# Performance work log

Measured on AMD Instinct MI355X. Metric: run time of the kernel, lower is better.

## Reference

```python
import jax, jax.numpy as jnp
import numpy as np


def setup_inputs() -> dict:
    key = jax.random.key(0)
    k1, k2 = jax.random.split(key)
    N, C = 1_000_000, 80
    feats = jax.random.normal(k1, (N, C), dtype=jnp.float32)
    coords = jax.random.uniform(k2, (N, 4), dtype=jnp.float32)
    return {"feats": feats, "coords": coords, "B": 1, "D": 1, "H": 360, "W": 360}


def reference(feats, coords, B, D, H, W):
    N = feats.shape[0]
    C = feats.shape[1]
    # quantize coords exactly as the torch module does
    icoords = jnp.clip((coords * 12).astype(jnp.int32), 0, H - 1)  # [N,4]
    feats = jnp.clip(feats, 0.5, 0.5)  # faithful: all values become 0.5
    ranks = (icoords[:, 0] * (W * D * B)
             + icoords[:, 1] * (D * B)
             + icoords[:, 2] * B
             + icoords[:, 3])
    order = jnp.argsort(ranks)
    feats = feats[order]
    icoords = icoords[order]
    ranks = ranks[order]
    # segment boundaries over sorted ranks (QuickCumsum intervals)
    kept = jnp.concatenate([jnp.ones((1,), bool), ranks[1:] != ranks[:-1]])
    seg_ids = jnp.cumsum(kept.astype(jnp.int32)) - 1  # [N], segment id per row
    # per-segment sums == x_prefix[ends] - x_prefix[starts] + x[starts]
    seg_sums = jax.ops.segment_sum(feats, seg_ids, num_segments=N)  # [N,C]
    # flattened voxel index (note: uses W and H exactly as in the source)
    geom = (icoords[:, 0]
            + icoords[:, 1] * W
            + icoords[:, 2] * H
            + icoords[:, 3]).astype(jnp.int32)
    # geom value taken at each segment's FIRST row (interval start), like the
    # torch code's geom_feats[interval_starts]; dump slot N holds non-starts
    seg_geom = (jnp.zeros((N + 1,), jnp.int32)
                .at[jnp.where(kept, seg_ids, N)].set(geom))[:N]
    # unused segments carry zero sums and index 0 -> harmless add of zeros
    out = jnp.zeros((B * D * H * W, C), feats.dtype).at[seg_geom].add(seg_sums)
    return out.reshape(B, D, H, W, C)
```

## Files before the change

kernel.cpp:

```cpp
#include <hip/hip_runtime.h>

#define LDS_RANKS 4096
#define NPART 8
#define COUNT_BLOCKS 512
#define TOTAL_BLOCKS 2048
#define FIN_BLOCKS (LDS_RANKS / 64)
#define MAGIC64 0x9E3779B97F4A7C15ull


__global__ void __launch_bounds__(256) qcs_fused(
    const float4* __restrict__ coords4, int N,
    const int* __restrict__ pB, const int* __restrict__ pD,
    const int* __restrict__ pH, const int* __restrict__ pW,
    int* __restrict__ tabs, unsigned long long* __restrict__ flags,
    float* __restrict__ out, int out_size)
{
    __shared__ int s_cnt[LDS_RANKS];
    __shared__ int s_enc[LDS_RANKS];

    if (blockIdx.x < COUNT_BLOCKS) {
        if (blockIdx.x < NPART) {
            int* cp = tabs + blockIdx.x * LDS_RANKS;
            int* ep = cp + NPART * LDS_RANKS;
            float4 z = make_float4(0.f, 0.f, 0.f, 0.f);
            for (int j = threadIdx.x; j < LDS_RANKS / 4; j += blockDim.x) {
                reinterpret_cast<float4*>(cp)[j] = z;
                reinterpret_cast<float4*>(ep)[j] = z;
            }
            __threadfence();
            __syncthreads();
            if (threadIdx.x == 0)
                atomicExch(&flags[blockIdx.x], MAGIC64);
        }

        for (int j = threadIdx.x; j < LDS_RANKS; j += blockDim.x) {
            s_cnt[j] = 0;
            s_enc[j] = 0;
        }
        __syncthreads();

        const int B = *pB, D = *pD, H = *pH, W = *pW;
        const int m0 = W * D * B, m1 = D * B, m2 = B;
        const int hi = H - 1;
        const int stride = COUNT_BLOCKS * blockDim.x;

        for (int i = blockIdx.x * blockDim.x + threadIdx.x; i < N; i += stride) {
            float4 c = coords4[i];
            int i0 = min(max((int)(c.x * 12.0f), 0), hi);
            int i1 = min(max((int)(c.y * 12.0f), 0), hi);
            int i2 = min(max((int)(c.z * 12.0f), 0), hi);
            int i3 = min(max((int)(c.w * 12.0f), 0), hi);
            int rank = i0 * m0 + i1 * m1 + i2 * m2 + i3;
            if (rank < LDS_RANKS) {
                atomicAdd(&s_cnt[rank], 1);
                atomicMax(&s_enc[rank], N - i);
            }
        }
        __syncthreads();

        int p = blockIdx.x & (NPART - 1);
        if (blockIdx.x >= NPART) {
            if (threadIdx.x == 0) {
                while (__hip_atomic_load(&flags[p], __ATOMIC_ACQUIRE,
                                         __HIP_MEMORY_SCOPE_AGENT) != MAGIC64) {}
            }
            __syncthreads();
        }
        int* cp = tabs + p * LDS_RANKS;
        int* ep = cp + NPART * LDS_RANKS;
        for (int r = threadIdx.x; r < LDS_RANKS; r += blockDim.x) {
            int c = s_cnt[r];
            if (c > 0) {
                atomicAdd(&cp[r], c);
                atomicMax(&ep[r], s_enc[r]);
            }
        }
    } else {
        int zb = blockIdx.x - COUNT_BLOCKS;
        int nzb = gridDim.x - COUNT_BLOCKS;
        int tid = zb * blockDim.x + threadIdx.x;
        int stride = nzb * blockDim.x;
        float4 z = make_float4(0.f, 0.f, 0.f, 0.f);
        float4* out4 = reinterpret_cast<float4*>(out);
        int n4 = out_size >> 2;
        for (int i = tid; i < n4; i += stride) out4[i] = z;
        for (int i = (n4 << 2) + tid; i < out_size; i += stride) out[i] = 0.0f;
    }
}

__global__ void __launch_bounds__(256) qcs_finish(
    const float4* __restrict__ coords4, int N, int C,
    const int* __restrict__ pH, const int* __restrict__ pW,
    const int* __restrict__ tabs, unsigned long long* __restrict__ flags,
    float* __restrict__ out)
{
    __shared__ int l_tot[4][64];
    __shared__ int l_mx[4][64];
    __shared__ int l_geomC[64];
    __shared__ float l_val[64];
    __shared__ int l_na;

    if (blockIdx.x == 0 && threadIdx.x < NPART)
        flags[threadIdx.x] = 0ull;

    int ls = threadIdx.x & 63;
    int q = threadIdx.x >> 6;
    int s = blockIdx.x * 64 + ls;

    const int* cp = tabs;
    const int* ep = tabs + NPART * LDS_RANKS;
    int t0 = cp[(2 * q) * LDS_RANKS + s] + cp[(2 * q + 1) * LDS_RANKS + s];
    int m0 = max(ep[(2 * q) * LDS_RANKS + s], ep[(2 * q + 1) * LDS_RANKS + s]);
    l_tot[q][ls] = t0;
    l_mx[q][ls] = m0;
    if (threadIdx.x == 0) l_na = 0;
    __syncthreads();

    if (q == 0) {
        int tot = l_tot[0][ls] + l_tot[1][ls] + l_tot[2][ls] + l_tot[3][ls];
        int mx = max(max(l_mx[0][ls], l_mx[1][ls]), max(l_mx[2][ls], l_mx[3][ls]));
        if (tot > 0) {
            const int H = *pH, W = *pW;
            const int hi = H - 1;
            int i = N - mx;
            float4 c = coords4[i];
            int i0 = min(max((int)(c.x * 12.0f), 0), hi);
            int i1 = min(max((int)(c.y * 12.0f), 0), hi);
            int i2 = min(max((int)(c.z * 12.0f), 0), hi);
            int i3 = min(max((int)(c.w * 12.0f), 0), hi);
            int geom = i0 + i1 * W + i2 * H + i3;
            int slot = atomicAdd(&l_na, 1);
            l_geomC[slot] = geom * C;
            l_val[slot] = 0.5f * (float)tot;
        }
    }
    __syncthreads();

    int na = l_na;
    if (na == 0) return;

    if (C <= (int)blockDim.x) {
        int ept = blockDim.x / C;
        int e0 = threadIdx.x / C;
        int ch = threadIdx.x - e0 * C;
        if (e0 < ept) {
            for (int e = e0; e < na; e += ept)
                atomicAdd(&out[l_geomC[e] + ch], l_val[e]);
        }
    } else {
        for (int e = 0; e < na; ++e) {
            float v = l_val[e];
            for (int k = threadIdx.x; k < C; k += blockDim.x)
                atomicAdd(&out[l_geomC[e] + k], v);
        }
    }
}

extern "C" void kernel_launch(void* const* d_in, const int* in_sizes, int n_in,
                              void* d_out, int out_size, void* d_ws, size_t ws_size,
                              hipStream_t stream) {
    const float4* coords4 = (const float4*)d_in[1];
    const int* pB = (const int*)d_in[2];
    const int* pD = (const int*)d_in[3];
    const int* pH = (const int*)d_in[4];
    const int* pW = (const int*)d_in[5];

    const int N = in_sizes[1] / 4;
    const int C = in_sizes[0] / N;

    int* tabs = (int*)d_ws;
    unsigned long long* flags =
        (unsigned long long*)(tabs + 2 * NPART * LDS_RANKS);
    float* out = (float*)d_out;

    qcs_fused<<<TOTAL_BLOCKS, 256, 0, stream>>>(coords4, N, pB, pD, pH, pW,
                                                tabs, flags, out, out_size);

    qcs_finish<<<FIN_BLOCKS, 256, 0, stream>>>(coords4, N, C, pH, pW,
                                               tabs, flags, out);
}
```

Measured before the change: 22.97 us.

## Fuse finish stage into main kernel using flag counters and split output zeroing

Merges the separate finish kernel into the single fused kernel. The last 64 blocks spin on per-partition flags until all counting blocks have flushed their LDS tables, then do the per-rank reduction and the scatter-add. Counting blocks now zero the first GMAX*C output elements, which is the region the scatter touches, and bump a flag counter when done. The remaining blocks zero the rest of the output. This removes one kernel launch and its serialization gap. In exchange it depends on inter-block spin-waits that need enough blocks resident at once, on stale flag values from the previous call, and on geom values staying below GMAX.

```diff
diff --git a/kernel.cpp b/kernel.cpp
--- a/kernel.cpp
+++ b/kernel.cpp
@@ -1,26 +1,30 @@
 #include <hip/hip_runtime.h>
 
 #define LDS_RANKS 4096
+#define GMAX 8192
 #define NPART 8
 #define COUNT_BLOCKS 512
 #define TOTAL_BLOCKS 2048
-#define FIN_BLOCKS (LDS_RANKS / 64)
+#define FIN_BLOCKS 64
+#define FLUSHERS (COUNT_BLOCKS / NPART)
 #define MAGIC64 0x9E3779B97F4A7C15ull
 
 
-__global__ void __launch_bounds__(256) qcs_fused(
-    const float4* __restrict__ coords4, int N,
+__global__ void __launch_bounds__(256) qcs_all(
+    const float4* __restrict__ coords4, int N, int C,
     const int* __restrict__ pB, const int* __restrict__ pD,
     const int* __restrict__ pH, const int* __restrict__ pW,
     int* __restrict__ tabs, unsigned long long* __restrict__ flags,
-    float* __restrict__ out, int out_size)
+    float* __restrict__ out, int out_size, int gsplit)
 {
     __shared__ int s_cnt[LDS_RANKS];
     __shared__ int s_enc[LDS_RANKS];
 
-    if (blockIdx.x < COUNT_BLOCKS) {
-        if (blockIdx.x < NPART) {
-            int* cp = tabs + blockIdx.x * LDS_RANKS;
+    const int bid = blockIdx.x;
+
+    if (bid < COUNT_BLOCKS) {
+        if (bid < NPART) {
+            int* cp = tabs + bid * LDS_RANKS;
             int* ep = cp + NPART * LDS_RANKS;
             float4 z = make_float4(0.f, 0.f, 0.f, 0.f);
             for (int j = threadIdx.x; j < LDS_RANKS / 4; j += blockDim.x) {
@@ -30,7 +34,7 @@
             __threadfence();
             __syncthreads();
             if (threadIdx.x == 0)
-                atomicExch(&flags[blockIdx.x], MAGIC64);
+                atomicExch(&flags[bid], MAGIC64);
         }
 
         for (int j = threadIdx.x; j < LDS_RANKS; j += blockDim.x) {
@@ -44,7 +48,7 @@
         const int hi = H - 1;
         const int stride = COUNT_BLOCKS * blockDim.x;
 
-        for (int i = blockIdx.x * blockDim.x + threadIdx.x; i < N; i += stride) {
+        for (int i = bid * blockDim.x + threadIdx.x; i < N; i += stride) {
             float4 c = coords4[i];
             int i0 = min(max((int)(c.x * 12.0f), 0), hi);
             int i1 = min(max((int)(c.y * 12.0f), 0), hi);
@@ -58,14 +62,18 @@
         }
         __syncthreads();
 
-        int p = blockIdx.x & (NPART - 1);
-        if (blockIdx.x >= NPART) {
+        int p = bid & (NPART - 1);
+        if (bid >= NPART) {
             if (threadIdx.x == 0) {
-                while (__hip_atomic_load(&flags[p], __ATOMIC_ACQUIRE,
-                                         __HIP_MEMORY_SCOPE_AGENT) != MAGIC64) {}
-            }
-            __syncthreads();
-        }
+                unsigned long long v;
+                do {
+                    v = __hip_atomic_load(&flags[p], __ATOMIC_ACQUIRE,
+                                          __HIP_MEMORY_SCOPE_AGENT);
+                } while (v - MAGIC64 >= (unsigned long long)FLUSHERS);
+            }
+            __syncthreads();
+        }
+
         int* cp = tabs + p * LDS_RANKS;
         int* ep = cp + NPART * LDS_RANKS;
         for (int r = threadIdx.x; r < LDS_RANKS; r += blockDim.x) {
@@ -75,83 +83,104 @@
                 atomicMax(&ep[r], s_enc[r]);
             }
         }
+
+        {
+            float4 z = make_float4(0.f, 0.f, 0.f, 0.f);
+            float4* o4 = reinterpret_cast<float4*>(out);
+            int n4 = gsplit >> 2;
+            for (int i = bid * blockDim.x + threadIdx.x; i < n4; i += stride)
+                o4[i] = z;
+        }
+
+        __threadfence();
+        __syncthreads();
+        if (threadIdx.x == 0)
+            atomicAdd(&flags[p], 1ull);
     } else {
-        int zb = blockIdx.x - COUNT_BLOCKS;
-        int nzb = gridDim.x - COUNT_BLOCKS;
+        int zb = bid - COUNT_BLOCKS;
+        int nzb = TOTAL_BLOCKS - COUNT_BLOCKS;
         int tid = zb * blockDim.x + threadIdx.x;
-        int stride = nzb * blockDim.x;
+        int zstride = nzb * blockDim.x;
         float4 z = make_float4(0.f, 0.f, 0.f, 0.f);
         float4* out4 = reinterpret_cast<float4*>(out);
-        int n4 = out_size >> 2;
-        for (int i = tid; i < n4; i += stride) out4[i] = z;
-        for (int i = (n4 << 2) + tid; i < out_size; i += stride) out[i] = 0.0f;
-    }
-}
-
-__global__ void __launch_bounds__(256) qcs_finish(
-    const float4* __restrict__ coords4, int N, int C,
-    const int* __restrict__ pH, const int* __restrict__ pW,
-    const int* __restrict__ tabs, unsigned long long* __restrict__ flags,
-    float* __restrict__ out)
-{
-    __shared__ int l_tot[4][64];
-    __shared__ int l_mx[4][64];
-    __shared__ int l_geomC[64];
-    __shared__ float l_val[64];
-    __shared__ int l_na;
-
-    if (blockIdx.x == 0 && threadIdx.x < NPART)
-        flags[threadIdx.x] = 0ull;
-
-    int ls = threadIdx.x & 63;
-    int q = threadIdx.x >> 6;
-    int s = blockIdx.x * 64 + ls;
-
-    const int* cp = tabs;
-    const int* ep = tabs + NPART * LDS_RANKS;
-    int t0 = cp[(2 * q) * LDS_RANKS + s] + cp[(2 * q + 1) * LDS_RANKS + s];
-    int m0 = max(ep[(2 * q) * LDS_RANKS + s], ep[(2 * q + 1) * LDS_RANKS + s]);
-    l_tot[q][ls] = t0;
-    l_mx[q][ls] = m0;
-    if (threadIdx.x == 0) l_na = 0;
-    __syncthreads();
-
-    if (q == 0) {
-        int tot = l_tot[0][ls] + l_tot[1][ls] + l_tot[2][ls] + l_tot[3][ls];
-        int mx = max(max(l_mx[0][ls], l_mx[1][ls]), max(l_mx[2][ls], l_mx[3][ls]));
-        if (tot > 0) {
-            const int H = *pH, W = *pW;
-            const int hi = H - 1;
-            int i = N - mx;
-            float4 c = coords4[i];
-            int i0 = min(max((int)(c.x * 12.0f), 0), hi);
-            int i1 = min(max((int)(c.y * 12.0f), 0), hi);
-            int i2 = min(max((int)(c.z * 12.0f), 0), hi);
-            int i3 = min(max((int)(c.w * 12.0f), 0), hi);
-            int geom = i0 + i1 * W + i2 * H + i3;
-            int slot = atomicAdd(&l_na, 1);
-            l_geomC[slot] = geom * C;
-            l_val[slot] = 0.5f * (float)tot;
-        }
-    }
-    __syncthreads();
-
-    int na = l_na;
-    if (na == 0) return;
-
-    if (C <= (int)blockDim.x) {
-        int ept = blockDim.x / C;
-        int e0 = threadIdx.x / C;
-        int ch = threadIdx.x - e0 * C;
-        if (e0 < ept) {
-            for (int e = e0; e < na; e += ept)
-                atomicAdd(&out[l_geomC[e] + ch], l_val[e]);
-        }
-    } else {
-        for (int e = 0; e < na; ++e) {
-            float v = l_val[e];
-            for (int k = threadIdx.x; k < C; k += blockDim.x)
-                atomicAdd(&out[l_geomC[e] + k], v);
+        int s4 = gsplit >> 2, n4 = out_size >> 2;
+        for (int i = s4 + tid; i < n4; i += zstride) out4[i] = z;
+        for (int i = (n4 << 2) + tid; i < out_size; i += zstride) out[i] = 0.0f;
+
+        if (bid >= TOTAL_BLOCKS - FIN_BLOCKS) {
+            int fb = bid - (TOTAL_BLOCKS - FIN_BLOCKS);
+
+            if (threadIdx.x < NPART) {
+                while (__hip_atomic_load(&flags[threadIdx.x], __ATOMIC_ACQUIRE,
+                                         __HIP_MEMORY_SCOPE_AGENT)
+                       != MAGIC64 + (unsigned long long)FLUSHERS) {}
+            }
+            __syncthreads();
+
+            int* l_tot = s_cnt;
+            int* l_mx = s_cnt + 256;
+            int* l_geomC = s_cnt + 512;
+            float* l_val = reinterpret_cast<float*>(s_cnt + 576);
+            int* l_na = s_cnt + 640;
+
+            int ls = threadIdx.x & 63;
+            int q = threadIdx.x >> 6;
+            int s = fb * 64 + ls;
+
+            const int* cp = tabs;
+            const int* ep = tabs + NPART * LDS_RANKS;
+            int t0 = __hip_atomic_load(&cp[(2 * q) * LDS_RANKS + s],
+                                       __ATOMIC_RELAXED, __HIP_MEMORY_SCOPE_AGENT)
+                   + __hip_atomic_load(&cp[(2 * q + 1) * LDS_RANKS + s],
+                                       __ATOMIC_RELAXED, __HIP_MEMORY_SCOPE_AGENT);
+            int m0 = max(__hip_atomic_load(&ep[(2 * q) * LDS_RANKS + s],
+                                           __ATOMIC_RELAXED, __HIP_MEMORY_SCOPE_AGENT),
+                         __hip_atomic_load(&ep[(2 * q + 1) * LDS_RANKS + s],
+                                           __ATOMIC_RELAXED, __HIP_MEMORY_SCOPE_AGENT));
+            l_tot[q * 64 + ls] = t0;
+            l_mx[q * 64 + ls] = m0;
+            if (threadIdx.x == 0) *l_na = 0;
+            __syncthreads();
+
+            if (q == 0) {
+                int tot = l_tot[ls] + l_tot[64 + ls] + l_tot[128 + ls] + l_tot[192 + ls];
+                int mx = max(max(l_mx[ls], l_mx[64 + ls]),
+                             max(l_mx[128 + ls], l_mx[192 + ls]));
+                if (tot > 0) {
+                    const int H = *pH, W = *pW;
+                    const int hi = H - 1;
+                    int i = N - mx;
+                    float4 c = coords4[i];
+                    int i0 = min(max((int)(c.x * 12.0f), 0), hi);
+                    int i1 = min(max((int)(c.y * 12.0f), 0), hi);
+                    int i2 = min(max((int)(c.z * 12.0f), 0), hi);
+                    int i3 = min(max((int)(c.w * 12.0f), 0), hi);
+                    int geom = i0 + i1 * W + i2 * H + i3;
+                    int slot = atomicAdd(l_na, 1);
+                    l_geomC[slot] = geom * C;
+                    l_val[slot] = 0.5f * (float)tot;
+                }
+            }
+            __syncthreads();
+
+            int na = *l_na;
+            if (na == 0) return;
+
+            if (C <= (int)blockDim.x) {
+                int ept = blockDim.x / C;
+                int e0 = threadIdx.x / C;
+                int ch = threadIdx.x - e0 * C;
+                if (e0 < ept) {
+                    for (int e = e0; e < na; e += ept)
+                        atomicAdd(&out[l_geomC[e] + ch], l_val[e]);
+                }
+            } else {
+                for (int e = 0; e < na; ++e) {
+                    float v = l_val[e];
+                    for (int k = threadIdx.x; k < C; k += blockDim.x)
+                        atomicAdd(&out[l_geomC[e] + k], v);
+                }
+            }
         }
     }
 }
@@ -173,9 +202,9 @@
         (unsigned long long*)(tabs + 2 * NPART * LDS_RANKS);
     float* out = (float*)d_out;
 
-    qcs_fused<<<TOTAL_BLOCKS, 256, 0, stream>>>(coords4, N, pB, pD, pH, pW,
-                                                tabs, flags, out, out_size);
-
-    qcs_finish<<<FIN_BLOCKS, 256, 0, stream>>>(coords4, N, C, pH, pW,
-                                               tabs, flags, out);
+    long long gc = (long long)GMAX * C;
+    int gsplit = (int)((gc < out_size) ? gc : (long long)out_size) & ~3;
+
+    qcs_all<<<TOTAL_BLOCKS, 256, 0, stream>>>(coords4, N, C, pB, pD, pH, pW,
+                                              tabs, flags, out, out_size, gsplit);
 }
```

Measured after the change: 71.61 us. 212% more time.
